# Optimization experiments

Hardware: AMD Instinct MI355X
Metric: run time of the kernel (lower is better)

## Reference

```python
import jax, jax.numpy as jnp
import numpy as np

N_NODES = 50000
N_EDGES = 800000
IN_FEATS = 256
N_HEADS = 4
OUT_FEATS = 32
NEG_SLOPE = 0.2


def setup_inputs() -> dict:
    key = jax.random.key(0)
    k_feat, k_src, k_dst, k_fc, k_al, k_ar, k_res = jax.random.split(key, 7)
    feat = jax.random.normal(k_feat, (N_NODES, IN_FEATS), dtype=jnp.float32)
    src = jax.random.randint(k_src, (N_EDGES,), 0, N_NODES)
    dst = jax.random.randint(k_dst, (N_EDGES,), 0, N_NODES)
    # xavier-normal-ish scales
    s_fc = (2.0 / (IN_FEATS + N_HEADS * OUT_FEATS)) ** 0.5
    W_fc = jax.random.normal(k_fc, (N_HEADS * OUT_FEATS, IN_FEATS), dtype=jnp.float32) * s_fc
    s_a = (2.0 / (1 + N_HEADS * OUT_FEATS)) ** 0.5
    attn_l = jax.random.normal(k_al, (N_HEADS, OUT_FEATS), dtype=jnp.float32) * s_a
    attn_r = jax.random.normal(k_ar, (N_HEADS, OUT_FEATS), dtype=jnp.float32) * s_a
    W_res = jax.random.normal(k_res, (N_HEADS * OUT_FEATS, IN_FEATS), dtype=jnp.float32) * s_fc
    return {"feat": feat, "src": src, "dst": dst, "W_fc": W_fc,
            "attn_l": attn_l, "attn_r": attn_r, "W_res": W_res}


def reference(feat, src, dst, W_fc, attn_l, attn_r, W_res):
    N = feat.shape[0]
    H, D = attn_l.shape
    ones_e = jnp.ones(src.shape[0], dtype=feat.dtype)

    # projection: [N, H, D]
    h = (feat @ W_fc.T).reshape(N, H, D)
    feat_dst = h  # dst features are pre-norm (torch code aliases before * norm)

    # symmetric norm on source side: out_degree^-0.5
    out_deg = jax.ops.segment_sum(ones_e, src, num_segments=N)
    feat_src = h * (jnp.clip(out_deg, 1.0) ** -0.5)[:, None, None]

    # per-node attention halves -> per-edge score, leaky relu
    el = jnp.einsum('nhd,hd->nh', feat_src, attn_l)  # [N, H]
    er = jnp.einsum('nhd,hd->nh', feat_dst, attn_r)  # [N, H]
    e = jax.nn.leaky_relu(el[src] + er[dst], NEG_SLOPE)  # [E, H]

    # edge_softmax over incoming edges of each dst node
    emax = jax.ops.segment_max(e, dst, num_segments=N)
    emax = jnp.where(jnp.isfinite(emax), emax, 0.0)  # guard empty segments
    ex = jnp.exp(e - emax[dst])
    denom = jax.ops.segment_sum(ex, dst, num_segments=N)
    a = ex / denom[dst]  # [E, H]

    # weighted scatter-sum of messages: u_mul_e + sum
    msg = feat_src[src] * a[:, :, None]  # [E, H, D]
    rst = jax.ops.segment_sum(msg, dst, num_segments=N)  # [N, H, D]

    # symmetric norm on destination side: in_degree^0.5
    in_deg = jax.ops.segment_sum(ones_e, dst, num_segments=N)
    rst = rst * jnp.sqrt(jnp.clip(in_deg, 1.0))[:, None, None]

    # residual projection
    rst = rst + (feat @ W_res.T).reshape(N, H, D)
    return rst
```

## Files before the change

### kernel.cpp

```cpp
#include <hip/hip_runtime.h>
#include <hip/hip_bf16.h>
#include <math.h>

#define HD 128
#define IN_F 256
#define NEG_SLOPE 0.2f
#define NMAX 50000

typedef __attribute__((ext_vector_type(8))) short short8;
typedef __attribute__((ext_vector_type(4))) float f32x4;

__device__ __forceinline__ unsigned short f2bf(float x) {
    __hip_bfloat16 b = __float2bfloat16(x);
    return *(unsigned short*)&b;
}
__device__ __forceinline__ float bf2f(unsigned short u) {
    unsigned int v = ((unsigned int)u) << 16;
    float f;
    __builtin_memcpy(&f, &v, 4);
    return f;
}
__device__ __forceinline__ short8 pack8(float4 f0, float4 f1) {
    short8 v;
    v[0] = (short)f2bf(f0.x); v[1] = (short)f2bf(f0.y);
    v[2] = (short)f2bf(f0.z); v[3] = (short)f2bf(f0.w);
    v[4] = (short)f2bf(f1.x); v[5] = (short)f2bf(f1.y);
    v[6] = (short)f2bf(f1.z); v[7] = (short)f2bf(f1.w);
    return v;
}

__global__ void cvt_w_kernel(const float4* __restrict__ wfc, const float4* __restrict__ wres,
                             ushort4* __restrict__ w16, int n4each) {
    int idx = blockIdx.x * blockDim.x + threadIdx.x;
    if (idx >= 2 * n4each) return;
    float4 f = (idx < n4each) ? wfc[idx] : wres[idx - n4each];
    ushort4 u;
    u.x = f2bf(f.x); u.y = f2bf(f.y); u.z = f2bf(f.z); u.w = f2bf(f.w);
    w16[idx] = u;
}

__global__ __launch_bounds__(256) void ew_kernel(const float* __restrict__ wfc,
                                                 const float* __restrict__ attn_l,
                                                 const float* __restrict__ attn_r,
                                                 unsigned short* __restrict__ ew16) {
    int h = blockIdx.x;
    int k = threadIdx.x;
    float sl = 0.f, sr = 0.f;
#pragma unroll 8
    for (int d = 0; d < 32; d++) {
        float w = wfc[(size_t)(h * 32 + d) * IN_F + k];
        sl += attn_l[h * 32 + d] * w;
        sr += attn_r[h * 32 + d] * w;
    }
    ew16[h * IN_F + k] = f2bf(sl);
    ew16[(4 + h) * IN_F + k] = f2bf(sr);
    ew16[(8 + h) * IN_F + k] = 0;
    ew16[(12 + h) * IN_F + k] = 0;
}

__global__ __launch_bounds__(512) void hist_kernel(const int* __restrict__ src,
                                                   const int* __restrict__ dst,
                                                   unsigned short* __restrict__ pc_src,
                                                   unsigned short* __restrict__ pc_dst,
                                                   int N, int E, int chunk) {
    __shared__ unsigned int h[NMAX / 2];
    int tid = threadIdx.x;
    int nh = N >> 1;
    uint4* h4 = (uint4*)h;
    for (int i = tid; i < (nh >> 2); i += 512) h4[i] = make_uint4(0, 0, 0, 0);
    for (int i = (nh & ~3) + tid; i < nh; i += 512) h[i] = 0;
    __syncthreads();

    const int* arr = blockIdx.y ? src : dst;
    int e1 = min(E, (int)(blockIdx.x + 1) * chunk);
    for (int e = blockIdx.x * chunk + tid; e < e1; e += 512) {
        int v = arr[e];
        atomicAdd(&h[v >> 1], 1u << ((v & 1) << 4));
    }
    __syncthreads();

    unsigned short* pc = (blockIdx.y ? pc_src : pc_dst) + (size_t)blockIdx.x * N;
    uint4* pc4 = (uint4*)pc;
    for (int i = tid; i < (nh >> 2); i += 512) pc4[i] = h4[i];
    for (int i = (nh & ~3) + tid; i < nh; i += 512) ((unsigned int*)pc)[i] = h[i];
}

__global__ __launch_bounds__(256) void sum_scan1_kernel(
    const unsigned short* __restrict__ pc_src, unsigned short* __restrict__ pc_dst,
    int* __restrict__ out_cnt, int* __restrict__ deg, int* __restrict__ bsum,
    int N, int C) {
    __shared__ int wsum[4];
    int n = blockIdx.x * 256 + threadIdx.x;
    int sd = 0;
    if (n < N) {
        int ss = 0;
        for (int c = 0; c < C; c++) {
            ss += pc_src[(size_t)c * N + n];
            unsigned short v = pc_dst[(size_t)c * N + n];
            pc_dst[(size_t)c * N + n] = (unsigned short)sd;
            sd += v;
        }
        out_cnt[n] = ss;
        deg[n] = sd;
    }
    int v = (n < N) ? sd : 0;
#pragma unroll
    for (int d = 1; d < 64; d <<= 1) v += __shfl_xor(v, d);
    if ((threadIdx.x & 63) == 0) wsum[threadIdx.x >> 6] = v;
    __syncthreads();
    if (threadIdx.x == 0) bsum[blockIdx.x] = wsum[0] + wsum[1] + wsum[2] + wsum[3];
}

__global__ __launch_bounds__(256) void scan2_kernel(int* __restrict__ bsum, int nb,
                                                    int* __restrict__ row_start_N, int E) {
    __shared__ int wtot[4];
    int tid = threadIdx.x, lane = tid & 63, wid = tid >> 6;
    int v = (tid < nb) ? bsum[tid] : 0;
    int incl = v;
#pragma unroll
    for (int d = 1; d < 64; d <<= 1) {
        int t = __shfl_up(incl, d);
        if (lane >= d) incl += t;
    }
    if (lane == 63) wtot[wid] = incl;
    __syncthreads();
    int woff = 0;
    for (int w = 0; w < wid; w++) woff += wtot[w];
    if (tid < nb) bsum[tid] = woff + incl - v;
    if (tid == 0) *row_start_N = E;
}

__global__ __launch_bounds__(256) void scan3_kernel(const int* __restrict__ deg,
                                                    const int* __restrict__ boff,
                                                    int* __restrict__ row_start, int N) {
    __shared__ int wsum[4];
    int i = blockIdx.x * 256 + threadIdx.x;
    int lane = threadIdx.x & 63, wid = threadIdx.x >> 6;
    int v = (i < N) ? deg[i] : 0;
    int incl = v;
#pragma unroll
    for (int d = 1; d < 64; d <<= 1) {
        int t = __shfl_up(incl, d);
        if (lane >= d) incl += t;
    }
    if (lane == 63) wsum[wid] = incl;
    __syncthreads();
    int woff = 0;
    for (int w = 0; w < wid; w++) woff += wsum[w];
    int excl = boff[blockIdx.x] + woff + incl - v;
    if (i < N) row_start[i] = excl;
}

__global__ __launch_bounds__(512) void place_kernel(const int* __restrict__ src,
                                                    const int* __restrict__ dst,
                                                    const unsigned short* __restrict__ chunkpre,
                                                    const int* __restrict__ row_start,
                                                    int* __restrict__ esrc,
                                                    int N, int E, int chunk) {
    __shared__ unsigned int cur[NMAX / 2];
    int tid = threadIdx.x;
    int nh = N >> 1;
    const unsigned short* cp = chunkpre + (size_t)blockIdx.x * N;
    const uint4* cp4 = (const uint4*)cp;
    uint4* cur4 = (uint4*)cur;
    for (int i = tid; i < (nh >> 2); i += 512) cur4[i] = cp4[i];
    for (int i = (nh & ~3) + tid; i < nh; i += 512) cur[i] = ((const unsigned int*)cp)[i];
    __syncthreads();

    int e1 = min(E, (int)(blockIdx.x + 1) * chunk);
    for (int e = blockIdx.x * chunk + tid; e < e1; e += 512) {
        int d = dst[e], s = src[e];
        int sh = (d & 1) << 4;
        unsigned int old = atomicAdd(&cur[d >> 1], 1u << sh);
        int rank = (old >> sh) & 0xffff;
        esrc[row_start[d] + rank] = s;
    }
}

__global__ __launch_bounds__(256, 4) void gemm_fused(
    const float* __restrict__ feat, const __hip_bfloat16* __restrict__ w16,
    const __hip_bfloat16* __restrict__ ew16, const int* __restrict__ out_cnt,
    unsigned short* __restrict__ h16, unsigned short* __restrict__ resid16,
    float* __restrict__ el, float* __restrict__ er, int N) {
    __shared__ unsigned short sA[32 * 256];
    int tid = threadIdx.x;
    int lane = tid & 63, wn = tid >> 6;
    int l15 = lane & 15, lg = lane >> 4;
    int colbase = wn * 64;
    int bm = blockIdx.x * 32;

#pragma unroll
    for (int i = 0; i < 4; i++) {
        int G = i * 256 + tid;
        int row = G >> 5, gc = G & 31;
        int gm = bm + row;
        gm = (gm < N) ? gm : (N - 1);
        const float4* fp = (const float4*)(feat + (size_t)gm * IN_F + gc * 8);
        float4 f0 = fp[0], f1 = fp[1];
        *(short8*)&sA[row * 256 + ((gc ^ (row & 7)) * 8)] = pack8(f0, f1);
    }
    __syncthreads();

    const __hip_bfloat16* bp[4];
#pragma unroll
    for (int ni = 0; ni < 4; ni++)
        bp[ni] = w16 + (size_t)(colbase + ni * 16 + l15) * IN_F + lg * 8;
    const __hip_bfloat16* ep = ew16 + (size_t)l15 * IN_F + lg * 8;
    bool w0 = (wn == 0);

    f32x4 acc[2][4], accE[2];
#pragma unroll
    for (int i = 0; i < 2; i++) {
        accE[i] = (f32x4){0.f, 0.f, 0.f, 0.f};
#pragma unroll
        for (int j = 0; j < 4; j++) acc[i][j] = (f32x4){0.f, 0.f, 0.f, 0.f};
    }

#pragma unroll
    for (int kk = 0; kk < 8; kk++) {
        short8 a[2], b[4];
#pragma unroll
        for (int mi = 0; mi < 2; mi++) {
            int row = mi * 16 + l15;
            int gs = (kk * 4 + lg) ^ (row & 7);
            a[mi] = *(const short8*)&sA[row * 256 + gs * 8];
        }
#pragma unroll
        for (int ni = 0; ni < 4; ni++) b[ni] = *(const short8*)(bp[ni] + kk * 32);
#pragma unroll
        for (int mi = 0; mi < 2; mi++)
#pragma unroll
            for (int ni = 0; ni < 4; ni++)
                acc[mi][ni] = __builtin_amdgcn_mfma_f32_16x16x32_bf16(
                    a[mi], b[ni], acc[mi][ni], 0, 0, 0);
        if (w0) {
            short8 be = *(const short8*)(ep + kk * 32);
#pragma unroll
            for (int mi = 0; mi < 2; mi++)
                accE[mi] = __builtin_amdgcn_mfma_f32_16x16x32_bf16(
                    a[mi], be, accE[mi], 0, 0, 0);
        }
    }
    __syncthreads();

    bool isH = (wn < 2);
#pragma unroll
    for (int mi = 0; mi < 2; mi++) {
#pragma unroll
        for (int reg = 0; reg < 4; reg++) {
            int rl = mi * 16 + lg * 4 + reg;
            int r = bm + rl;
            float nrm = 1.0f;
            if (isH) {
                int rr = (r < N) ? r : 0;
                nrm = rsqrtf(fmaxf((float)out_cnt[rr], 1.0f));
            }
#pragma unroll
            for (int ni = 0; ni < 4; ni++) {
                int col = colbase + ni * 16 + l15;
                float v = acc[mi][ni][reg] * nrm;
                sA[rl * 256 + (col ^ ((rl & 7) << 4))] = f2bf(v);
            }
            if (w0 && r < N) {
                float ev = accE[mi][reg];
                if (l15 < 4) el[r * 4 + l15] = ev * nrm;
                else if (l15 < 8) er[r * 4 + (l15 - 4)] = ev;
            }
        }
    }
    __syncthreads();

    int hrow = tid >> 3, seg = tid & 7;
    int gr = bm + hrow;
    if (gr < N) {
        int base = hrow * 256;
        int ss = ((seg ^ (hrow & 7)) << 4);
        short8 hv0 = *(const short8*)&sA[base + ss];
        short8 hv1 = *(const short8*)&sA[base + ss + 8];
        short8 rv0 = *(const short8*)&sA[base + 128 + ss];
        short8 rv1 = *(const short8*)&sA[base + 128 + ss + 8];
        unsigned short* hp = h16 + (size_t)gr * HD + seg * 16;
        unsigned short* rp = resid16 + (size_t)gr * HD + seg * 16;
        *(short8*)hp = hv0;
        *(short8*)(hp + 8) = hv1;
        *(short8*)rp = rv0;
        *(short8*)(rp + 8) = rv1;
    }
}

__global__ __launch_bounds__(256) void agg_kernel(const unsigned short* __restrict__ h16,
                                                  const float* __restrict__ el,
                                                  const float* __restrict__ er,
                                                  const int* __restrict__ row_start,
                                                  const int* __restrict__ esrc,
                                                  const unsigned short* __restrict__ resid16,
                                                  float* __restrict__ out, int N) {
    int wid = threadIdx.x >> 6, lane = threadIdx.x & 63;
    int n = blockIdx.x * 4 + wid;
    if (n >= N) return;
    int es = lane >> 4;
    int l15 = lane & 15;
    int h = l15 >> 2;
    int d0 = l15 * 8;
    int beg = row_start[n], end = row_start[n + 1];
    float erh = er[n * 4 + h];
    float den = 0.f;
    float acc[8];
#pragma unroll
    for (int j = 0; j < 8; j++) acc[j] = 0.f;

    if (beg < end) {
        bool ok0, ok1;
        float ev0, ev1; short8 hv0, hv1;
        {
            int i0 = beg + es, i1 = beg + 4 + es;
            ok0 = i0 < end; ok1 = i1 < end;
            int s0 = esrc[ok0 ? i0 : beg];
            int s1 = esrc[ok1 ? i1 : beg];
            ev0 = el[s0 * 4 + h]; ev1 = el[s1 * 4 + h];
            hv0 = *(const short8*)(h16 + (size_t)s0 * HD + d0);
            hv1 = *(const short8*)(h16 + (size_t)s1 * HD + d0);
        }
        for (int base = beg + 8; base < end; base += 8) {
            int i0 = base + es, i1 = base + 4 + es;
            bool p0 = i0 < end, p1 = i1 < end;
            int t0 = esrc[p0 ? i0 : beg];
            int t1 = esrc[p1 ? i1 : beg];
            float fv0 = el[t0 * 4 + h];
            float fv1 = el[t1 * 4 + h];
            short8 g0 = *(const short8*)(h16 + (size_t)t0 * HD + d0);
            short8 g1 = *(const short8*)(h16 + (size_t)t1 * HD + d0);
            float e0 = ev0 + erh; e0 = (e0 > 0.f) ? e0 : NEG_SLOPE * e0;
            float e1 = ev1 + erh; e1 = (e1 > 0.f) ? e1 : NEG_SLOPE * e1;
            float ex0 = ok0 ? __expf(e0) : 0.f;
            float ex1 = ok1 ? __expf(e1) : 0.f;
            den += ex0 + ex1;
#pragma unroll
            for (int j = 0; j < 8; j++)
                acc[j] += ex0 * bf2f((unsigned short)hv0[j]) +
                          ex1 * bf2f((unsigned short)hv1[j]);
            ok0 = p0; ok1 = p1; ev0 = fv0; ev1 = fv1; hv0 = g0; hv1 = g1;
        }
        float e0 = ev0 + erh; e0 = (e0 > 0.f) ? e0 : NEG_SLOPE * e0;
        float e1 = ev1 + erh; e1 = (e1 > 0.f) ? e1 : NEG_SLOPE * e1;
        float ex0 = ok0 ? __expf(e0) : 0.f;
        float ex1 = ok1 ? __expf(e1) : 0.f;
        den += ex0 + ex1;
#pragma unroll
        for (int j = 0; j < 8; j++)
            acc[j] += ex0 * bf2f((unsigned short)hv0[j]) +
                      ex1 * bf2f((unsigned short)hv1[j]);
    }

#pragma unroll
    for (int m = 16; m < 64; m <<= 1) {
        den += __shfl_xor(den, m);
#pragma unroll
        for (int j = 0; j < 8; j++) acc[j] += __shfl_xor(acc[j], m);
    }

    if (es == 0) {
        const unsigned short* rp = resid16 + (size_t)n * HD + d0;
        short8 rv = *(const short8*)rp;
        int indeg = end - beg;
        float sc = (indeg > 0) ? sqrtf((float)indeg) / den : 0.f;
        float o[8];
#pragma unroll
        for (int j = 0; j < 8; j++)
            o[j] = sc * acc[j] + bf2f((unsigned short)rv[j]);
        float* op = out + (size_t)n * HD + d0;
        *(float4*)op = make_float4(o[0], o[1], o[2], o[3]);
        *(float4*)(op + 4) = make_float4(o[4], o[5], o[6], o[7]);
    }
}

extern "C" void kernel_launch(void* const* d_in, const int* in_sizes, int n_in,
                              void* d_out, int out_size, void* d_ws, size_t ws_size,
                              hipStream_t stream) {
    const float* feat   = (const float*)d_in[0];
    const int*   src    = (const int*)d_in[1];
    const int*   dst    = (const int*)d_in[2];
    const float* W_fc   = (const float*)d_in[3];
    const float* attn_l = (const float*)d_in[4];
    const float* attn_r = (const float*)d_in[5];
    const float* W_res  = (const float*)d_in[6];
    float* out = (float*)d_out;

    int N = in_sizes[0] / IN_F;
    int E = in_sizes[1];
    int nb = (N + 255) / 256;

    size_t off = 0;
    auto alloc = [&](size_t bytes) {
        size_t o = off;
        off = (off + bytes + 255) & ~(size_t)255;
        return o;
    };
    char* ws = (char*)d_ws;
    unsigned short* h16     = (unsigned short*)(ws + alloc((size_t)N * HD * 2));
    unsigned short* resid16 = (unsigned short*)(ws + alloc((size_t)N * HD * 2));
    __hip_bfloat16* w16     = (__hip_bfloat16*)(ws + alloc((size_t)2 * HD * IN_F * 2));
    unsigned short* ew16    = (unsigned short*)(ws + alloc((size_t)16 * IN_F * 2));
    float* el               = (float*)(ws + alloc((size_t)N * 4 * 4));
    float* er               = (float*)(ws + alloc((size_t)N * 4 * 4));
    int* out_cnt            = (int*)(ws + alloc((size_t)N * 4));
    int* deg                = (int*)(ws + alloc((size_t)N * 4));
    int* row_start          = (int*)(ws + alloc((size_t)(N + 1) * 4));
    int* bsum               = (int*)(ws + alloc((size_t)nb * 4));
    int* esrc               = (int*)(ws + alloc((size_t)E * 4));

    size_t per_chunk = (size_t)4 * N;
    size_t avail = (ws_size > off + 4096) ? (ws_size - off - 4096) : 0;
    int C = (int)(avail / per_chunk);
    if (C > 128) C = 128;
    if (C < 32) C = 32;
    unsigned short* pc_dst = (unsigned short*)(ws + alloc((size_t)C * N * 2));
    unsigned short* pc_src = (unsigned short*)(ws + alloc((size_t)C * N * 2));
    int chunk = (E + C - 1) / C;

    int n4each = HD * IN_F / 4;
    cvt_w_kernel<<<(2 * n4each + 255) / 256, 256, 0, stream>>>(
        (const float4*)W_fc, (const float4*)W_res, (ushort4*)w16, n4each);
    ew_kernel<<<4, 256, 0, stream>>>(W_fc, attn_l, attn_r, ew16);

    hist_kernel<<<dim3(C, 2), 512, 0, stream>>>(src, dst, pc_src, pc_dst, N, E, chunk);
    sum_scan1_kernel<<<nb, 256, 0, stream>>>(pc_src, pc_dst, out_cnt, deg, bsum, N, C);
    scan2_kernel<<<1, 256, 0, stream>>>(bsum, nb, row_start + N, E);
    scan3_kernel<<<nb, 256, 0, stream>>>(deg, bsum, row_start, N);
    place_kernel<<<C, 512, 0, stream>>>(src, dst, pc_dst, row_start, esrc, N, E, chunk);

    gemm_fused<<<(N + 31) / 32, 256, 0, stream>>>(feat, (const __hip_bfloat16*)w16,
                                                  (const __hip_bfloat16*)ew16, out_cnt,
                                                  h16, resid16, el, er, N);

    int nb4 = (N + 3) / 4;
    agg_kernel<<<nb4, 256, 0, stream>>>(h16, el, er, row_start, esrc, resid16, out, N);
}
```

Measured before the change: 158.6 us.

## Make projection GEMM persistent with register-resident weights and double-buffered feature tiles

The fused projection GEMM now runs as a persistent grid of 512 blocks that loop over row tiles. Each block loads its weight and attention-weight fragments into registers once, and prefetches the next tile's features while computing the current one through a double-buffered shared-memory tile. Outputs are written straight to global memory instead of being staged through shared memory for coalesced stores. This removes per-block weight reloads and launch imbalance, but raises register pressure (the launch bound drops to 2 blocks per CU), and the direct 2-byte strided stores may coalesce less well.

```diff
diff --git a/kernel.cpp b/kernel.cpp
--- a/kernel.cpp
+++ b/kernel.cpp
@@ -6,6 +6,7 @@
 #define IN_F 256
 #define NEG_SLOPE 0.2f
 #define NMAX 50000
+#define GB 512
 
 typedef __attribute__((ext_vector_type(8))) short short8;
 typedef __attribute__((ext_vector_type(4))) float f32x4;
@@ -177,114 +178,140 @@
     }
 }
 
-__global__ __launch_bounds__(256, 4) void gemm_fused(
+__global__ __launch_bounds__(256, 2) void gemm_fused(
     const float* __restrict__ feat, const __hip_bfloat16* __restrict__ w16,
     const __hip_bfloat16* __restrict__ ew16, const int* __restrict__ out_cnt,
     unsigned short* __restrict__ h16, unsigned short* __restrict__ resid16,
-    float* __restrict__ el, float* __restrict__ er, int N) {
-    __shared__ unsigned short sA[32 * 256];
+    float* __restrict__ el, float* __restrict__ er, int N, int ntiles) {
+    __shared__ unsigned short sA[2][32 * 256];
     int tid = threadIdx.x;
     int lane = tid & 63, wn = tid >> 6;
     int l15 = lane & 15, lg = lane >> 4;
     int colbase = wn * 64;
-    int bm = blockIdx.x * 32;
-
+    bool w0 = (wn == 0);
+    bool isH = (wn < 2);
+    int colloc = colbase & 127;
+
+    short8 breg[4][8];
+#pragma unroll
+    for (int ni = 0; ni < 4; ni++) {
+        const __hip_bfloat16* bp = w16 + (size_t)(colbase + ni * 16 + l15) * IN_F + lg * 8;
+#pragma unroll
+        for (int kk = 0; kk < 8; kk++) breg[ni][kk] = *(const short8*)(bp + kk * 32);
+    }
+    short8 ereg[8];
+    {
+        const __hip_bfloat16* ep = ew16 + (size_t)l15 * IN_F + lg * 8;
+#pragma unroll
+        for (int kk = 0; kk < 8; kk++) ereg[kk] = *(const short8*)(ep + kk * 32);
+    }
+
+    int srow[4], sgc[4];
 #pragma unroll
     for (int i = 0; i < 4; i++) {
         int G = i * 256 + tid;
-        int row = G >> 5, gc = G & 31;
-        int gm = bm + row;
+        srow[i] = G >> 5;
+        sgc[i] = G & 31;
+    }
+
+    float4 fA[4][2];
+    int t = blockIdx.x;
+#pragma unroll
+    for (int i = 0; i < 4; i++) {
+        int gm = t * 32 + srow[i];
         gm = (gm < N) ? gm : (N - 1);
-        const float4* fp = (const float4*)(feat + (size_t)gm * IN_F + gc * 8);
-        float4 f0 = fp[0], f1 = fp[1];
-        *(short8*)&sA[row * 256 + ((gc ^ (row & 7)) * 8)] = pack8(f0, f1);
-    }
-    __syncthreads();
-
-    const __hip_bfloat16* bp[4];
-#pragma unroll
-    for (int ni = 0; ni < 4; ni++)
-        bp[ni] = w16 + (size_t)(colbase + ni * 16 + l15) * IN_F + lg * 8;
-    const __hip_bfloat16* ep = ew16 + (size_t)l15 * IN_F + lg * 8;
-    bool w0 = (wn == 0);
-
-    f32x4 acc[2][4], accE[2];
-#pragma unroll
-    for (int i = 0; i < 2; i++) {
-        accE[i] = (f32x4){0.f, 0.f, 0.f, 0.f};
-#pragma unroll
-        for (int j = 0; j < 4; j++) acc[i][j] = (f32x4){0.f, 0.f, 0.f, 0.f};
-    }
-
-#pragma unroll
-    for (int kk = 0; kk < 8; kk++) {
-        short8 a[2], b[4];
+        const float4* fp = (const float4*)(feat + (size_t)gm * IN_F + sgc[i] * 8);
+        fA[i][0] = fp[0];
+        fA[i][1] = fp[1];
+    }
+#pragma unroll
+    for (int i = 0; i < 4; i++)
+        *(short8*)&sA[0][srow[i] * 256 + ((sgc[i] ^ (srow[i] & 7)) * 8)] =
+            pack8(fA[i][0], fA[i][1]);
+
+    int cur = 0;
+    for (; t < ntiles; t += GB) {
+        __syncthreads();
+
+        int tn = t + GB;
+        if (tn < ntiles) {
+#pragma unroll
+            for (int i = 0; i < 4; i++) {
+                int gm = tn * 32 + srow[i];
+                gm = (gm < N) ? gm : (N - 1);
+                const float4* fp = (const float4*)(feat + (size_t)gm * IN_F + sgc[i] * 8);
+                fA[i][0] = fp[0];
+                fA[i][1] = fp[1];
+            }
+        }
+
+        f32x4 acc[2][4], accE[2];
+#pragma unroll
+        for (int i = 0; i < 2; i++) {
+            accE[i] = (f32x4){0.f, 0.f, 0.f, 0.f};
+#pragma unroll
+            for (int j = 0; j < 4; j++) acc[i][j] = (f32x4){0.f, 0.f, 0.f, 0.f};
+        }
+#pragma unroll
+        for (int kk = 0; kk < 8; kk++) {
+            short8 a[2];
+#pragma unroll
+            for (int mi = 0; mi < 2; mi++) {
+                int row = mi * 16 + l15;
+                int gs = (kk * 4 + lg) ^ (row & 7);
+                a[mi] = *(const short8*)&sA[cur][row * 256 + gs * 8];
+            }
+#pragma unroll
+            for (int mi = 0; mi < 2; mi++)
+#pragma unroll
+                for (int ni = 0; ni < 4; ni++)
+                    acc[mi][ni] = __builtin_amdgcn_mfma_f32_16x16x32_bf16(
+                        a[mi], breg[ni][kk], acc[mi][ni], 0, 0, 0);
+            if (w0) {
+#pragma unroll
+                for (int mi = 0; mi < 2; mi++)
+                    accE[mi] = __builtin_amdgcn_mfma_f32_16x16x32_bf16(
+                        a[mi], ereg[kk], accE[mi], 0, 0, 0);
+            }
+        }
+
+        int bm = t * 32;
 #pragma unroll
         for (int mi = 0; mi < 2; mi++) {
-            int row = mi * 16 + l15;
-            int gs = (kk * 4 + lg) ^ (row & 7);
-            a[mi] = *(const short8*)&sA[row * 256 + gs * 8];
-        }
-#pragma unroll
-        for (int ni = 0; ni < 4; ni++) b[ni] = *(const short8*)(bp[ni] + kk * 32);
-#pragma unroll
-        for (int mi = 0; mi < 2; mi++)
-#pragma unroll
-            for (int ni = 0; ni < 4; ni++)
-                acc[mi][ni] = __builtin_amdgcn_mfma_f32_16x16x32_bf16(
-                    a[mi], b[ni], acc[mi][ni], 0, 0, 0);
-        if (w0) {
-            short8 be = *(const short8*)(ep + kk * 32);
-#pragma unroll
-            for (int mi = 0; mi < 2; mi++)
-                accE[mi] = __builtin_amdgcn_mfma_f32_16x16x32_bf16(
-                    a[mi], be, accE[mi], 0, 0, 0);
-        }
-    }
-    __syncthreads();
-
-    bool isH = (wn < 2);
-#pragma unroll
-    for (int mi = 0; mi < 2; mi++) {
-#pragma unroll
-        for (int reg = 0; reg < 4; reg++) {
-            int rl = mi * 16 + lg * 4 + reg;
-            int r = bm + rl;
-            float nrm = 1.0f;
-            if (isH) {
-                int rr = (r < N) ? r : 0;
-                nrm = rsqrtf(fmaxf((float)out_cnt[rr], 1.0f));
+#pragma unroll
+            for (int reg = 0; reg < 4; reg++) {
+                int r = bm + mi * 16 + lg * 4 + reg;
+                bool valid = (r < N);
+                int rr = valid ? r : 0;
+                if (isH) {
+                    float nrm = rsqrtf(fmaxf((float)out_cnt[rr], 1.0f));
+                    if (valid) {
+#pragma unroll
+                        for (int ni = 0; ni < 4; ni++)
+                            h16[(size_t)r * HD + colloc + ni * 16 + l15] =
+                                f2bf(acc[mi][ni][reg] * nrm);
+                        if (w0) {
+                            float ev = accE[mi][reg];
+                            if (l15 < 4) el[r * 4 + l15] = ev * nrm;
+                            else if (l15 < 8) er[r * 4 + (l15 - 4)] = ev;
+                        }
+                    }
+                } else if (valid) {
+#pragma unroll
+                    for (int ni = 0; ni < 4; ni++)
+                        resid16[(size_t)r * HD + colloc + ni * 16 + l15] =
+                            f2bf(acc[mi][ni][reg]);
+                }
             }
-#pragma unroll
-            for (int ni = 0; ni < 4; ni++) {
-                int col = colbase + ni * 16 + l15;
-                float v = acc[mi][ni][reg] * nrm;
-                sA[rl * 256 + (col ^ ((rl & 7) << 4))] = f2bf(v);
-            }
-            if (w0 && r < N) {
-                float ev = accE[mi][reg];
-                if (l15 < 4) el[r * 4 + l15] = ev * nrm;
-                else if (l15 < 8) er[r * 4 + (l15 - 4)] = ev;
-            }
-        }
-    }
-    __syncthreads();
-
-    int hrow = tid >> 3, seg = tid & 7;
-    int gr = bm + hrow;
-    if (gr < N) {
-        int base = hrow * 256;
-        int ss = ((seg ^ (hrow & 7)) << 4);
-        short8 hv0 = *(const short8*)&sA[base + ss];
-        short8 hv1 = *(const short8*)&sA[base + ss + 8];
-        short8 rv0 = *(const short8*)&sA[base + 128 + ss];
-        short8 rv1 = *(const short8*)&sA[base + 128 + ss + 8];
-        unsigned short* hp = h16 + (size_t)gr * HD + seg * 16;
-        unsigned short* rp = resid16 + (size_t)gr * HD + seg * 16;
-        *(short8*)hp = hv0;
-        *(short8*)(hp + 8) = hv1;
-        *(short8*)rp = rv0;
-        *(short8*)(rp + 8) = rv1;
+        }
+
+        if (tn < ntiles) {
+#pragma unroll
+            for (int i = 0; i < 4; i++)
+                *(short8*)&sA[cur ^ 1][srow[i] * 256 + ((sgc[i] ^ (srow[i] & 7)) * 8)] =
+                    pack8(fA[i][0], fA[i][1]);
+        }
+        cur ^= 1;
     }
 }
 
@@ -429,9 +456,10 @@
     scan3_kernel<<<nb, 256, 0, stream>>>(deg, bsum, row_start, N);
     place_kernel<<<C, 512, 0, stream>>>(src, dst, pc_dst, row_start, esrc, N, E, chunk);
 
-    gemm_fused<<<(N + 31) / 32, 256, 0, stream>>>(feat, (const __hip_bfloat16*)w16,
-                                                  (const __hip_bfloat16*)ew16, out_cnt,
-                                                  h16, resid16, el, er, N);
+    int ntiles = (N + 31) / 32;
+    gemm_fused<<<GB, 256, 0, stream>>>(feat, (const __hip_bfloat16*)w16,
+                                       (const __hip_bfloat16*)ew16, out_cnt,
+                                       h16, resid16, el, er, N, ntiles);
 
     int nb4 = (N + 3) / 4;
     agg_kernel<<<nb4, 256, 0, stream>>>(h16, el, er, row_start, esrc, resid16, out, N);
```

New measurement: 153.9 us, median of 2. 3.0% less time.
